# Optimization experiments

Hardware: AMD Instinct MI355X
Metric: run time of the kernel (lower is better)

## Reference

```python
import jax, jax.numpy as jnp
import numpy as np

N, E, D, B, C = 50000, 800000, 128, 20000, 40
EPS_BN = 1e-3    # keras BatchNormalization default epsilon
EPS_NRM = 1e-12  # keras ops.nn.normalize epsilon
FFN_DIMS = {"pre": (D, D), "c1p": (D, D), "c1u": (2 * D, D), "c2p": (D, D), "c2u": (2 * D, D), "post": (D, D)}


def setup_inputs() -> dict:
    key = jax.random.key(0)
    ks = jax.random.split(key, 8)
    inp = {
        "node_features": jax.random.normal(ks[0], (N, D), jnp.float32),
        "edges": jax.random.randint(ks[1], (2, E), 0, N, dtype=jnp.int32),
        "edge_w": jax.random.uniform(ks[2], (E,), jnp.float32),
        "input_node_idx": jax.random.randint(ks[3], (B,), 0, N, dtype=jnp.int32),
    }
    for i, (name, (din, dout)) in enumerate(FFN_DIMS.items()):
        kw = jax.random.fold_in(key, 100 + i)
        inp[name + "_g"] = jnp.ones((din,), jnp.float32)
        inp[name + "_be"] = jnp.zeros((din,), jnp.float32)
        inp[name + "_mu"] = jnp.zeros((din,), jnp.float32)
        inp[name + "_var"] = jnp.ones((din,), jnp.float32)
        inp[name + "_w"] = jax.random.normal(kw, (din, dout), jnp.float32) * (1.0 / float(np.sqrt(din)))
        inp[name + "_bi"] = jnp.zeros((dout,), jnp.float32)
    inp["logits_w"] = jax.random.normal(ks[4], (D, C), jnp.float32) * (1.0 / float(np.sqrt(D)))
    inp["logits_b"] = jnp.zeros((C,), jnp.float32)
    return inp


def ffn(x, g, be, mu, var, w, bi):
    # BatchNorm (inference running stats) -> Dropout (identity) -> Dense + exact gelu
    xn = (x - mu) * jax.lax.rsqrt(var + EPS_BN) * g + be
    return jax.nn.gelu(xn @ w + bi, approximate=False)


def l2norm(x):
    n = jnp.sqrt(jnp.sum(x * x, axis=-1, keepdims=True))
    return x / jnp.maximum(n, EPS_NRM)


def graph_conv(x, node_idx, nbr_idx, ew, prep, upd):
    # gather neighbours -> prepare FFN -> edge-weighted -> segment_sum (reduce='sum')
    msgs = ffn(x[nbr_idx], *prep) * ew[:, None]                         # [E, D]
    red = jax.ops.segment_sum(msgs, node_idx, num_segments=x.shape[0])  # [N, D]
    h = jnp.concatenate([x, red], axis=1)                               # [N, 2D] (combination='concat')
    return l2norm(ffn(h, *upd))                                         # normalize=True


def reference(node_features, edges, edge_w, input_node_idx,
              pre_g, pre_be, pre_mu, pre_var, pre_w, pre_bi,
              c1p_g, c1p_be, c1p_mu, c1p_var, c1p_w, c1p_bi,
              c1u_g, c1u_be, c1u_mu, c1u_var, c1u_w, c1u_bi,
              c2p_g, c2p_be, c2p_mu, c2p_var, c2p_w, c2p_bi,
              c2u_g, c2u_be, c2u_mu, c2u_var, c2u_w, c2u_bi,
              post_g, post_be, post_mu, post_var, post_w, post_bi,
              logits_w, logits_b):
    ew = edge_w / jnp.sum(edge_w)                       # edge_W normalized at init
    node_idx, nbr_idx = edges[0], edges[1]
    x = ffn(node_features, pre_g, pre_be, pre_mu, pre_var, pre_w, pre_bi)
    x = graph_conv(x, node_idx, nbr_idx, ew,
                   (c1p_g, c1p_be, c1p_mu, c1p_var, c1p_w, c1p_bi),
                   (c1u_g, c1u_be, c1u_mu, c1u_var, c1u_w, c1u_bi)) + x
    x = graph_conv(x, node_idx, nbr_idx, ew,
                   (c2p_g, c2p_be, c2p_mu, c2p_var, c2p_w, c2p_bi),
                   (c2u_g, c2u_be, c2u_mu, c2u_var, c2u_w, c2u_bi)) + x
    x = ffn(x, post_g, post_be, post_mu, post_var, post_w, post_bi)
    return x[input_node_idx] @ logits_w + logits_b      # [B, C]
```

## Files before the change

kernel.cpp:

```cpp
#include <hip/hip_runtime.h>
#include <hip/hip_fp16.h>
#include <math.h>

static constexpr int D = 128;
static constexpr int CAP = 64;
static constexpr float EPS_BN = 1e-3f;

typedef short short8 __attribute__((ext_vector_type(8)));
typedef short short4v __attribute__((ext_vector_type(4)));
typedef float float4v __attribute__((ext_vector_type(4)));

__device__ __forceinline__ float gelu_exact(float x) {
    return 0.5f * x * (1.0f + erff(x * 0.70710678118654752f));
}

__device__ __forceinline__ void f32_to_hilo(float f, short& h, short& l) {
    unsigned u = __float_as_uint(f);
    h = (short)(u >> 16);
    float hf = __uint_as_float(u & 0xFFFF0000u);
    unsigned lu = __float_as_uint(f - hf);
    l = (short)(lu >> 16);
}

__device__ __forceinline__ short f32_to_bf16_rne(float f) {
    unsigned u = __float_as_uint(f);
    u += 0x7FFFu + ((u >> 16) & 1u);
    return (short)(u >> 16);
}

__device__ __forceinline__ void cvt_hilo8(const float4& x, const float4& y, short8& h8, short8& l8) {
    short h, l;
    f32_to_hilo(x.x, h, l); h8[0] = h; l8[0] = l;
    f32_to_hilo(x.y, h, l); h8[1] = h; l8[1] = l;
    f32_to_hilo(x.z, h, l); h8[2] = h; l8[2] = l;
    f32_to_hilo(x.w, h, l); h8[3] = h; l8[3] = l;
    f32_to_hilo(y.x, h, l); h8[4] = h; l8[4] = l;
    f32_to_hilo(y.y, h, l); h8[5] = h; l8[5] = l;
    f32_to_hilo(y.z, h, l); h8[6] = h; l8[6] = l;
    f32_to_hilo(y.w, h, l); h8[7] = h; l8[7] = l;
}

__device__ __forceinline__ short8 cvt_rne8(const float4& x, const float4& y) {
    short8 r;
    r[0] = f32_to_bf16_rne(x.x); r[1] = f32_to_bf16_rne(x.y);
    r[2] = f32_to_bf16_rne(x.z); r[3] = f32_to_bf16_rne(x.w);
    r[4] = f32_to_bf16_rne(y.x); r[5] = f32_to_bf16_rne(y.y);
    r[6] = f32_to_bf16_rne(y.z); r[7] = f32_to_bf16_rne(y.w);
    return r;
}

struct FoldArgs {
    const float* g[6]; const float* be[6]; const float* mu[6];
    const float* var[6]; const float* w[6]; const float* bi[6];
    short* wh[6]; short* wl[6]; float* bp[6]; int K[6];
};

__global__ void k_build(const int* __restrict__ edges, const float* __restrict__ ew,
                        int* __restrict__ cnt, float* __restrict__ sums,
                        unsigned* __restrict__ cw, FoldArgs fa, int E, int N, int fillBlocks) {
    __shared__ float sm[4];
    const int tid = threadIdx.x;
    const int lane = tid & 63, wvi = tid >> 6;

    if ((int)blockIdx.x < fillBlocks) {
        const int g = blockIdx.x & 15;
        const int bid = blockIdx.x >> 4;
        const int gstride = (fillBlocks >> 4) * 256;
        const int N16 = (N + 15) >> 4;
        const int lo = g * N16;
        const int hi = min(lo + N16, N);
        float s = 0.f;
        for (int e = bid * 256 + tid; e < E; e += gstride) {
            int dst = edges[e];
            if (dst >= lo && dst < hi) {
                int src = edges[E + e];
                float w = ew[e];
                s += w;
                unsigned short wb = __half_as_ushort(__float2half(w));
                int idx = atomicAdd(&cnt[dst], 1);
                if (idx < CAP)
                    cw[(size_t)dst * CAP + idx] = ((unsigned)src << 16) | (unsigned)wb;
            }
        }
        for (int off = 32; off > 0; off >>= 1) s += __shfl_down(s, off, 64);
        if (lane == 0) sm[wvi] = s;
        __syncthreads();
        if (tid == 0) {
            float t = sm[0] + sm[1] + sm[2] + sm[3];
            if (t != 0.f) atomicAdd(sums, t);
        }
    } else {
        const int idx = blockIdx.x - fillBlocks;
        const int f = idx >> 7;
        const int c = idx & 127;
        const int K = fa.K[f];
        const float* g = fa.g[f]; const float* be = fa.be[f];
        const float* mu = fa.mu[f]; const float* var = fa.var[f];
        const float* w = fa.w[f]; const float* bi = fa.bi[f];
        short* wh = fa.wh[f]; short* wl = fa.wl[f]; float* bp = fa.bp[f];
        float part = 0.f;
        for (int k = tid; k < K; k += blockDim.x) {
            float a = g[k] / sqrtf(var[k] + EPS_BN);
            float wv = w[k * D + c];
            float prod = a * wv;
            short hh, ll;
            f32_to_hilo(prod, hh, ll);
            wh[c * K + k] = hh;
            wl[c * K + k] = ll;
            part += (be[k] - mu[k] * a) * wv;
        }
        for (int off = 32; off > 0; off >>= 1) part += __shfl_down(part, off, 64);
        if (lane == 0) sm[wvi] = part;
        __syncthreads();
        if (tid == 0) bp[c] = bi[c] + sm[0] + sm[1] + sm[2] + sm[3];
    }
}

__device__ __forceinline__ void accum8(float* acc, const float4& raw, float w) {
    const __half2* hp = (const __half2*)&raw;
    #pragma unroll
    for (int t = 0; t < 4; t++) {
        float2 f = __half22float2(hp[t]);
        acc[t * 2]     += w * f.x;
        acc[t * 2 + 1] += w * f.y;
    }
}

__global__ void k_reduce(const int* __restrict__ cnt, const unsigned* __restrict__ cw,
                         const float* __restrict__ sums, const __half* __restrict__ y,
                         float* __restrict__ red, int N) {
    int n = blockIdx.x * (blockDim.x >> 6) + (threadIdx.x >> 6);
    if (n >= N) return;
    float inv = 1.0f / sums[0];
    int lane = threadIdx.x & 63;
    int sub = lane >> 4;
    int q = lane & 15;
    int count = min(cnt[n], CAP);
    int start = n * CAP;
    int end = start + count;
    float acc[8] = {0.f, 0.f, 0.f, 0.f, 0.f, 0.f, 0.f, 0.f};
    int i = start + sub;
    for (; i + 12 < end; i += 16) {
        unsigned c0 = cw[i];
        unsigned c1 = cw[i + 4];
        unsigned c2 = cw[i + 8];
        unsigned c3 = cw[i + 12];
        float4 r0 = *((const float4*)(y + (size_t)(c0 >> 16) * D) + q);
        float4 r1 = *((const float4*)(y + (size_t)(c1 >> 16) * D) + q);
        float4 r2 = *((const float4*)(y + (size_t)(c2 >> 16) * D) + q);
        float4 r3 = *((const float4*)(y + (size_t)(c3 >> 16) * D) + q);
        float w0 = __half2float(__ushort_as_half((unsigned short)(c0 & 0xFFFFu))) * inv;
        float w1 = __half2float(__ushort_as_half((unsigned short)(c1 & 0xFFFFu))) * inv;
        float w2 = __half2float(__ushort_as_half((unsigned short)(c2 & 0xFFFFu))) * inv;
        float w3 = __half2float(__ushort_as_half((unsigned short)(c3 & 0xFFFFu))) * inv;
        accum8(acc, r0, w0);
        accum8(acc, r1, w1);
        accum8(acc, r2, w2);
        accum8(acc, r3, w3);
    }
    for (; i < end; i += 4) {
        unsigned c = cw[i];
        float4 r = *((const float4*)(y + (size_t)(c >> 16) * D) + q);
        float w = __half2float(__ushort_as_half((unsigned short)(c & 0xFFFFu))) * inv;
        accum8(acc, r, w);
    }
    #pragma unroll
    for (int t = 0; t < 8; t++) {
        acc[t] += __shfl_xor(acc[t], 16, 64);
        acc[t] += __shfl_xor(acc[t], 32, 64);
    }
    if (sub == 0) {
        float4 o0 = {acc[0], acc[1], acc[2], acc[3]};
        float4 o1 = {acc[4], acc[5], acc[6], acc[7]};
        *((float4*)(red + (size_t)n * D + q * 8)) = o0;
        *((float4*)(red + (size_t)n * D + q * 8 + 4)) = o1;
    }
}

template<int K, bool SPLIT3, bool L2RES, bool OUT16>
__global__ void __launch_bounds__(512) k_ffn(
    const float* __restrict__ A0, const float* __restrict__ A1,
    const short* __restrict__ Wh, const short* __restrict__ Wl,
    const float* __restrict__ bp, const float* __restrict__ resid,
    float* __restrict__ outf, __half* __restrict__ outh, int N)
{
    constexpr int NB = SPLIT3 ? 2 : 1;
    constexpr int WSZ = 128 * K;
    constexpr int NC = K / 64;
    __shared__ short Wlds[NB * WSZ];
    __shared__ float rsum[2][16][4];

    const int tid = threadIdx.x;

    constexpr int ITER = (NB * WSZ) / (512 * 8);
    #pragma unroll
    for (int it = 0; it < ITER; ++it) {
        int s = it * 4096 + tid * 8;
        int buf = s / WSZ;
        int rem = s - buf * WSZ;
        int c = rem / K;
        int kk = (rem & (K - 1)) ^ ((c & 7) << 3);
        const short* src = (buf ? Wl : Wh) + c * K + kk;
        *(short8*)&Wlds[s] = *(const short8*)src;
    }
    __syncthreads();

    const int lane = tid & 63;
    const int wv = tid >> 6;
    const int ssub = wv >> 2;
    const int wc = wv & 3;
    const int m = lane & 15;
    const int quad = lane >> 4;
    const int nstrips = (N + 15) >> 4;
    const int stride = gridDim.x * 2;
    const int base = blockIdx.x * 2 + ssub;

    auto body = [&](int strip, bool active) {
        int r = active ? strip * 16 + m : m;
        if (r >= N) r = N - 1;
        const float* pA0 = A0 + (size_t)r * D;
        const float* pA1 = (K == 256) ? (A1 + (size_t)r * D) : pA0;

        float4 a[2][4];
        {
            const float4* s4 = (const float4*)pA0 + quad * 2;
            a[0][0] = s4[0]; a[0][1] = s4[1]; a[0][2] = s4[8]; a[0][3] = s4[9];
        }
        {
            const float4* s4 = (const float4*)(pA0 + 64) + quad * 2;
            a[1][0] = s4[0]; a[1][1] = s4[1]; a[1][2] = s4[8]; a[1][3] = s4[9];
        }

        float4v acc[2];
        acc[0] = (float4v){0.f, 0.f, 0.f, 0.f};
        acc[1] = (float4v){0.f, 0.f, 0.f, 0.f};

        #pragma unroll
        for (int cc = 0; cc < NC; ++cc) {
            #pragma unroll
            for (int ks = 0; ks < 2; ++ks) {
                const int kk = cc * 64 + ks * 32 + quad * 8;
                short8 ah, al;
                if (SPLIT3) cvt_hilo8(a[cc & 1][ks * 2], a[cc & 1][ks * 2 + 1], ah, al);
                else        ah = cvt_rne8(a[cc & 1][ks * 2], a[cc & 1][ks * 2 + 1]);
                #pragma unroll
                for (int tj = 0; tj < 2; ++tj) {
                    const int c = wc * 32 + tj * 16 + m;
                    const int idx = c * K + (kk ^ ((c & 7) << 3));
                    short8 bh = *(const short8*)&Wlds[idx];
                    if (SPLIT3) {
                        short8 bl = *(const short8*)&Wlds[WSZ + idx];
                        acc[tj] = __builtin_amdgcn_mfma_f32_16x16x32_bf16(al, bh, acc[tj], 0, 0, 0);
                        acc[tj] = __builtin_amdgcn_mfma_f32_16x16x32_bf16(ah, bl, acc[tj], 0, 0, 0);
                    }
                    acc[tj] = __builtin_amdgcn_mfma_f32_16x16x32_bf16(ah, bh, acc[tj], 0, 0, 0);
                }
            }
            if (cc + 2 < NC) {
                const int n2 = cc + 2;
                const float* src = (K == 256 && n2 >= 2) ? pA1 : pA0;
                const int kb = (K == 256) ? ((n2 & 1) * 64) : (n2 * 64);
                const float4* s4 = (const float4*)(src + kb) + quad * 2;
                a[cc & 1][0] = s4[0]; a[cc & 1][1] = s4[1];
                a[cc & 1][2] = s4[8]; a[cc & 1][3] = s4[9];
            }
        }

        #pragma unroll
        for (int tj = 0; tj < 2; ++tj) {
            float bv = bp[wc * 32 + tj * 16 + m];
            #pragma unroll
            for (int r4 = 0; r4 < 4; ++r4)
                acc[tj][r4] = gelu_exact(acc[tj][r4] + bv);
        }

        if (L2RES) {
            float ss[4];
            #pragma unroll
            for (int r4 = 0; r4 < 4; ++r4) {
                float v = acc[0][r4] * acc[0][r4] + acc[1][r4] * acc[1][r4];
                v += __shfl_xor(v, 1, 64);
                v += __shfl_xor(v, 2, 64);
                v += __shfl_xor(v, 4, 64);
                v += __shfl_xor(v, 8, 64);
                ss[r4] = v;
            }
            if (m == 0) {
                #pragma unroll
                for (int r4 = 0; r4 < 4; ++r4) rsum[ssub][quad * 4 + r4][wc] = ss[r4];
            }
            __syncthreads();
            #pragma unroll
            for (int r4 = 0; r4 < 4; ++r4) {
                const int rib = quad * 4 + r4;
                float tot = rsum[ssub][rib][0] + rsum[ssub][rib][1]
                          + rsum[ssub][rib][2] + rsum[ssub][rib][3];
                float inv = 1.0f / fmaxf(sqrtf(tot), 1e-12f);
                int row = strip * 16 + rib;
                if (active && row < N) {
                    #pragma unroll
                    for (int tj = 0; tj < 2; ++tj) {
                        int col = wc * 32 + tj * 16 + m;
                        outf[(size_t)row * D + col] = acc[tj][r4] * inv + resid[(size_t)row * D + col];
                    }
                }
            }
            __syncthreads();
        } else {
            #pragma unroll
            for (int r4 = 0; r4 < 4; ++r4) {
                int row = strip * 16 + quad * 4 + r4;
                if (active && row < N) {
                    #pragma unroll
                    for (int tj = 0; tj < 2; ++tj) {
                        int col = wc * 32 + tj * 16 + m;
                        if (OUT16) outh[(size_t)row * D + col] = __float2half(acc[tj][r4]);
                        else       outf[(size_t)row * D + col] = acc[tj][r4];
                    }
                }
            }
        }
    };

    if (L2RES) {
        int rem = nstrips - blockIdx.x * 2;
        int nit = rem > 0 ? (rem + stride - 1) / stride : 0;
        for (int it = 0; it < nit; ++it) {
            int strip = base + it * stride;
            body(strip, strip < nstrips);
        }
    } else {
        for (int strip = base; strip < nstrips; strip += stride)
            body(strip, true);
    }
}

__global__ void k_logits(const float* __restrict__ x, const int* __restrict__ idx,
                         const float* __restrict__ LW, const float* __restrict__ lb,
                         float* __restrict__ out, int B) {
    int wid = blockIdx.x * 4 + (threadIdx.x >> 6);
    int lane = threadIdx.x & 63;
    if (wid >= B) return;
    int row = __builtin_amdgcn_readfirstlane(idx[wid]);
    if (lane >= 40) return;
    float acc = lb[lane];
    const float4* xr = (const float4*)(x + (size_t)row * D);
    #pragma unroll 4
    for (int k4 = 0; k4 < 32; k4++) {
        float4 xv = xr[k4];
        acc += xv.x * LW[(4 * k4 + 0) * 40 + lane];
        acc += xv.y * LW[(4 * k4 + 1) * 40 + lane];
        acc += xv.z * LW[(4 * k4 + 2) * 40 + lane];
        acc += xv.w * LW[(4 * k4 + 3) * 40 + lane];
    }
    out[(size_t)wid * 40 + lane] = acc;
}

extern "C" void kernel_launch(void* const* d_in, const int* in_sizes, int n_in,
                              void* d_out, int out_size, void* d_ws, size_t ws_size,
                              hipStream_t stream) {
    const float* node_features = (const float*)d_in[0];
    const int*   edges         = (const int*)d_in[1];
    const float* edge_w        = (const float*)d_in[2];
    const int*   input_idx     = (const int*)d_in[3];
    const int N = in_sizes[0] / D;
    const int E = in_sizes[2];
    const int B = in_sizes[3];

    const float* P[6][6];
    for (int f = 0; f < 6; f++)
        for (int q = 0; q < 6; q++)
            P[f][q] = (const float*)d_in[4 + f * 6 + q];
    const float* logits_w = (const float*)d_in[40];
    const float* logits_b = (const float*)d_in[41];

    float* ws = (float*)d_ws;
    size_t nd = (size_t)N * D;
    float* xA  = ws;
    float* y   = ws + nd;
    float* red = ws + 2 * nd;
    float* p   = ws + 3 * nd;
    __half* yh = (__half*)p; p += nd / 2;
    const int Ks[6] = {128, 128, 256, 128, 256, 128};
    short* Wh[6]; short* Wl[6]; float* Bp[6];
    {
        short* sp = (short*)p;
        for (int f = 0; f < 6; f++) {
            Wh[f] = sp; sp += (size_t)Ks[f] * D;
            Wl[f] = sp; sp += (size_t)Ks[f] * D;
        }
        p = (float*)sp;
    }
    for (int f = 0; f < 6; f++) { Bp[f] = p; p += D; }
    int* cnt    = (int*)p; p += N;
    float* sums = p; p += 2;
    unsigned* cw = (unsigned*)p; p += (size_t)N * CAP;

    FoldArgs fa;
    for (int f = 0; f < 6; f++) {
        fa.g[f] = P[f][0]; fa.be[f] = P[f][1]; fa.mu[f] = P[f][2];
        fa.var[f] = P[f][3]; fa.w[f] = P[f][4]; fa.bi[f] = P[f][5];
        fa.wh[f] = Wh[f]; fa.wl[f] = Wl[f]; fa.bp[f] = Bp[f]; fa.K[f] = Ks[f];
    }

    const int fillBlocks = 2048;
    hipMemsetAsync(cnt, 0, ((size_t)N + 2) * sizeof(int), stream);
    k_build<<<fillBlocks + 768, 256, 0, stream>>>(edges, edge_w, cnt, sums, cw, fa, E, N, fillBlocks);

    const int rb = (N + 3) / 4;
    const int g1 = 256;
    const int g2 = 512;
    const int g3 = 1024;

    k_ffn<128, true,  false, false><<<g2, 512, 0, stream>>>(node_features, nullptr, Wh[0], Wl[0], Bp[0], nullptr, xA, nullptr, N);
    k_ffn<128, false, false, true ><<<g3, 512, 0, stream>>>(xA, nullptr, Wh[1], Wl[1], Bp[1], nullptr, nullptr, yh, N);
    k_reduce<<<rb, 256, 0, stream>>>(cnt, cw, sums, yh, red, N);
    k_ffn<256, true,  true,  false><<<g1, 512, 0, stream>>>(xA, red, Wh[2], Wl[2], Bp[2], xA, y, nullptr, N);
    k_ffn<128, false, false, true ><<<g3, 512, 0, stream>>>(y, nullptr, Wh[3], Wl[3], Bp[3], nullptr, nullptr, yh, N);
    k_reduce<<<rb, 256, 0, stream>>>(cnt, cw, sums, yh, red, N);
    k_ffn<256, true,  true,  false><<<g1, 512, 0, stream>>>(y, red, Wh[4], Wl[4], Bp[4], y, xA, nullptr, N);
    k_ffn<128, true,  false, false><<<g2, 512, 0, stream>>>(xA, nullptr, Wh[5], Wl[5], Bp[5], nullptr, red, nullptr, N);
    k_logits<<<(B + 3) / 4, 256, 0, stream>>>(red, input_idx, logits_w, logits_b, (float*)d_out, B);
}
```

Before: 452.9 us.

## Fuse post FFN with logits and compute it only for selected rows

The final post FFN, previously run over all N nodes, is now fused with the logits projection and computed only for the B gathered rows. The weights and batchnorm fold are staged in LDS per block. This skips roughly 60% of the post-FFN work and removes a full N×D intermediate write. Separately, the edge-bucketing build kernel switches from 16 to 8 destination range groups and launches fewer extra fold blocks, which trades fewer redundant edge scans for more atomic contention per group. The fused FFN uses plain fp32 FMA instead of the split bf16 MFMA path.

```diff
diff --git a/kernel.cpp b/kernel.cpp
--- a/kernel.cpp
+++ b/kernel.cpp
@@ -63,12 +63,12 @@
     const int lane = tid & 63, wvi = tid >> 6;
 
     if ((int)blockIdx.x < fillBlocks) {
-        const int g = blockIdx.x & 15;
-        const int bid = blockIdx.x >> 4;
-        const int gstride = (fillBlocks >> 4) * 256;
-        const int N16 = (N + 15) >> 4;
-        const int lo = g * N16;
-        const int hi = min(lo + N16, N);
+        const int g = blockIdx.x & 7;
+        const int bid = blockIdx.x >> 3;
+        const int gstride = (fillBlocks >> 3) * 256;
+        const int N8 = (N + 7) >> 3;
+        const int lo = g * N8;
+        const int hi = min(lo + N8, N);
         float s = 0.f;
         for (int e = bid * 256 + tid; e < E; e += gstride) {
             int dst = edges[e];
@@ -335,25 +335,59 @@
     }
 }
 
-__global__ void k_logits(const float* __restrict__ x, const int* __restrict__ idx,
-                         const float* __restrict__ LW, const float* __restrict__ lb,
-                         float* __restrict__ out, int B) {
-    int wid = blockIdx.x * 4 + (threadIdx.x >> 6);
-    int lane = threadIdx.x & 63;
-    if (wid >= B) return;
-    int row = __builtin_amdgcn_readfirstlane(idx[wid]);
-    if (lane >= 40) return;
-    float acc = lb[lane];
-    const float4* xr = (const float4*)(x + (size_t)row * D);
-    #pragma unroll 4
-    for (int k4 = 0; k4 < 32; k4++) {
-        float4 xv = xr[k4];
-        acc += xv.x * LW[(4 * k4 + 0) * 40 + lane];
-        acc += xv.y * LW[(4 * k4 + 1) * 40 + lane];
-        acc += xv.z * LW[(4 * k4 + 2) * 40 + lane];
-        acc += xv.w * LW[(4 * k4 + 3) * 40 + lane];
-    }
-    out[(size_t)wid * 40 + lane] = acc;
+__global__ void __launch_bounds__(512) k_postlogits(
+    const float* __restrict__ xA,
+    const float* __restrict__ g, const float* __restrict__ be,
+    const float* __restrict__ mu, const float* __restrict__ var,
+    const float* __restrict__ w,  const float* __restrict__ bi,
+    const int* __restrict__ idx,
+    const float* __restrict__ LW, const float* __restrict__ lb,
+    float* __restrict__ out, int B)
+{
+    __shared__ float Ws[128][128];
+    __shared__ float LWs[128][40];
+    __shared__ float afs[128], mus[128], bes[128], bis[128], lbs[40];
+    __shared__ float rowb[8][128];
+    __shared__ float yb[8][128];
+
+    const int tid = threadIdx.x;
+    for (int i = tid; i < 128 * 128 / 4; i += 512)
+        ((float4*)&Ws[0][0])[i] = ((const float4*)w)[i];
+    for (int i = tid; i < 128 * 40 / 4; i += 512)
+        ((float4*)&LWs[0][0])[i] = ((const float4*)LW)[i];
+    if (tid < 128) {
+        afs[tid] = g[tid] * rsqrtf(var[tid] + EPS_BN);
+        mus[tid] = mu[tid]; bes[tid] = be[tid]; bis[tid] = bi[tid];
+    }
+    if (tid < 40) lbs[tid] = lb[tid];
+    __syncthreads();
+
+    const int lane = tid & 63;
+    const int wv = tid >> 6;
+    const int nw = gridDim.x * 8;
+    for (int i = blockIdx.x * 8 + wv; i < B; i += nw) {
+        int row = idx[i];
+        float2 xv = ((const float2*)(xA + (size_t)row * D))[lane];
+        int k0 = lane * 2;
+        rowb[wv][k0]     = (xv.x - mus[k0])     * afs[k0]     + bes[k0];
+        rowb[wv][k0 + 1] = (xv.y - mus[k0 + 1]) * afs[k0 + 1] + bes[k0 + 1];
+        float acc0 = bis[lane], acc1 = bis[lane + 64];
+        #pragma unroll 4
+        for (int k = 0; k < 128; ++k) {
+            float a = rowb[wv][k];
+            acc0 += a * Ws[k][lane];
+            acc1 += a * Ws[k][lane + 64];
+        }
+        yb[wv][lane]      = gelu_exact(acc0);
+        yb[wv][lane + 64] = gelu_exact(acc1);
+        if (lane < 40) {
+            float o = lbs[lane];
+            #pragma unroll 4
+            for (int c = 0; c < 128; ++c)
+                o += yb[wv][c] * LWs[c][lane];
+            out[(size_t)i * 40 + lane] = o;
+        }
+    }
 }
 
 extern "C" void kernel_launch(void* const* d_in, const int* in_sizes, int n_in,
@@ -405,7 +439,7 @@
 
     const int fillBlocks = 2048;
     hipMemsetAsync(cnt, 0, ((size_t)N + 2) * sizeof(int), stream);
-    k_build<<<fillBlocks + 768, 256, 0, stream>>>(edges, edge_w, cnt, sums, cw, fa, E, N, fillBlocks);
+    k_build<<<fillBlocks + 640, 256, 0, stream>>>(edges, edge_w, cnt, sums, cw, fa, E, N, fillBlocks);
 
     const int rb = (N + 3) / 4;
     const int g1 = 256;
@@ -419,6 +453,6 @@
     k_ffn<128, false, false, true ><<<g3, 512, 0, stream>>>(y, nullptr, Wh[3], Wl[3], Bp[3], nullptr, nullptr, yh, N);
     k_reduce<<<rb, 256, 0, stream>>>(cnt, cw, sums, yh, red, N);
     k_ffn<256, true,  true,  false><<<g1, 512, 0, stream>>>(y, red, Wh[4], Wl[4], Bp[4], y, xA, nullptr, N);
-    k_ffn<128, true,  false, false><<<g2, 512, 0, stream>>>(xA, nullptr, Wh[5], Wl[5], Bp[5], nullptr, red, nullptr, N);
-    k_logits<<<(B + 3) / 4, 256, 0, stream>>>(red, input_idx, logits_w, logits_b, (float*)d_out, B);
-}
+    k_postlogits<<<256, 512, 0, stream>>>(xA, P[5][0], P[5][1], P[5][2], P[5][3], P[5][4], P[5][5],
+                                          input_idx, logits_w, logits_b, (float*)d_out, B);
+}
```

Result: slower. 478.8 us (+5.7%).
